# Kernel tuning notes

Hardware: AMD Instinct MI355X
Metric: run time of the kernel (lower is better)

Reference implementation:

```python
import jax, jax.numpy as jnp
import numpy as np
import math

DIM = 512      # vMF embedding dim
B = 512        # batch
K = 10         # sample_size
C = 8192       # num_classes
L = 0.7        # kappa_confidence
T_REJ = 32     # fixed rejection-sampling tries (acceptance ~0.7 per try)


def _vmf_logc(k, dim=DIM):
    # Approximate log normalizer from the paper (approximate_logc=True path).
    nm14 = (dim - 1) / 4.0
    nm12 = (dim - 1) / 2.0
    np12 = (dim + 1) / 2.0
    sqrtm = jnp.sqrt(nm12 * nm12 + k * k)
    sqrtp = jnp.sqrt(np12 * np12 + k * k)
    return nm14 * (jnp.log(nm12 + sqrtm) + jnp.log(nm12 + sqrtp)) - 0.5 * (sqrtm + sqrtp)


def _split(params):
    # params layout: [log_probs(1), means(DIM), hidden_ik(1)] (single component).
    means = params[..., 1:1 + DIM]
    hidden_ik = params[..., -1]
    mu = means / jnp.linalg.norm(means, axis=-1, keepdims=True)
    kappa = 1.0 / jnp.exp(hidden_ik)  # positive(x) = exp(x) parametrization
    return mu, kappa


def _vmf_sample(key, mu, kappa, n):
    # Wood's algorithm, vectorized over (b, n) with fixed-count rejection.
    b, d = mu.shape
    kap = kappa[:, None]  # (b,1)
    bb = (-2.0 * kap + jnp.sqrt(4.0 * kap * kap + (d - 1) ** 2)) / (d - 1)
    x0 = (1.0 - bb) / (1.0 + bb)
    cc = kap * x0 + (d - 1) * jnp.log(1.0 - x0 * x0)
    kz, ku, kv = jax.random.split(key, 3)
    z = jax.random.beta(kz, (d - 1) / 2.0, (d - 1) / 2.0, (T_REJ, b, n))
    w = (1.0 - (1.0 + bb) * z) / (1.0 - (1.0 - bb) * z)  # (T,b,n)
    u = jax.random.uniform(ku, (T_REJ, b, n), minval=1e-10)
    acc = kap * w + (d - 1) * jnp.log(1.0 - x0 * w) - cc >= jnp.log(u)
    idx = jnp.argmax(acc, axis=0)  # first accepted try
    w_sel = jnp.take_along_axis(w, idx[None], axis=0)[0]  # (b,n)
    v = jax.random.normal(kv, (b, n, d))
    v = v - jnp.einsum('bnd,bd->bn', v, mu)[..., None] * mu[:, None, :]
    v = v / jnp.linalg.norm(v, axis=-1, keepdims=True)
    sin_t = jnp.sqrt(jnp.clip(1.0 - w_sel * w_sel, 0.0))
    return w_sel[..., None] * mu[:, None, :] + sin_t[..., None] * v  # (b,n,d)


def setup_inputs() -> dict:
    key = jax.random.key(0)
    kp, kw, kl = jax.random.split(key, 3)
    # Input distribution parameters: random means, hidden_ik ~ log(1/kappa) with realistic kappa.
    parameters = jax.random.normal(kp, (B, DIM + 2), dtype=jnp.float32)
    kappa0 = L / (1.0 - L * L) * (DIM - 1) / math.sqrt(DIM)  # ~31
    parameters = parameters.at[:, -1].set(0.1 * parameters[:, -1] - math.log(kappa0))
    # Class weight, built exactly as in __init__ (non-deterministic target).
    means = jax.random.normal(kw, (C, DIM), dtype=jnp.float32) * (L / (1.0 - L * L) * (DIM - 1) / math.sqrt(DIM))
    norm = jnp.linalg.norm(means, axis=-1, keepdims=True)
    hidden_ik = jnp.log(1.0 / norm)  # ipositive = log
    weight = jnp.concatenate([jnp.zeros((C, 1), jnp.float32), means, hidden_ik], axis=-1)
    log_scale = jnp.asarray(2.773, dtype=jnp.float32)
    labels = jax.random.randint(kl, (B,), 0, C)
    return {"parameters": parameters, "weight": weight, "log_scale": log_scale, "labels": labels}


def reference(parameters, weight, log_scale, labels):
    scale = jnp.exp(log_scale)
    mu_x, kappa_x = _split(parameters)   # (b,d), (b,)
    mu_w, kappa_w = _split(weight)       # (c,d), (c,)
    sample = _vmf_sample(jax.random.key(42), mu_x, kappa_x, K)  # (b,K,d)
    sample = sample / jnp.linalg.norm(sample, axis=-1, keepdims=True)
    # logmls(b,k,c): samples have concentration k1=scale; since all means are unit,
    # ||k1*m1 + k2*m2|| = sqrt(k1^2 + k2^2 + 2*k1*k2*cos) -> single GEMM over d.
    cos = jnp.einsum('bkd,cd->bkc', sample, mu_w)
    k1 = scale
    k2 = kappa_w
    kk = jnp.sqrt(k1 * k1 + k2 * k2 + 2.0 * k1 * (k2 * cos))  # (b,K,c)
    logmls = _vmf_logc(k1) + _vmf_logc(k2)[None, None, :] - _vmf_logc(kk)
    neg_logden = jax.scipy.special.logsumexp(logmls, axis=2) - _vmf_logc(scale)  # (b,K)
    neg_lognum = scale * jnp.einsum('bd,bd->b', mu_x, mu_w[labels])
    losses = neg_logden.mean(axis=1) - neg_lognum  # (b,)
    b = parameters.shape[0]
    logits = jnp.zeros((b, C), parameters.dtype).at[jnp.arange(b), labels].set(-losses)
    return logits
```

## Files before the change

kernel.cpp:

```cpp
#include <hip/hip_runtime.h>
#include <stdint.h>

#define DIMD 512
#define BATCH 512
#define KSAMP 10
#define NCLS 8192
#define TREJ 32

typedef float f32x4 __attribute__((ext_vector_type(4)));
typedef long l2 __attribute__((ext_vector_type(2)));

__device__ inline uint64_t sm64(uint64_t x) {
  x += 0x9E3779B97F4A7C15ull;
  x = (x ^ (x >> 30)) * 0xBF58476D1CE4E5B9ull;
  x = (x ^ (x >> 27)) * 0x94D049BB133111EBull;
  return x ^ (x >> 31);
}
__device__ inline float u01(uint32_t u) {
  return ((float)u + 0.5f) * 2.3283064365386963e-10f;
}
__device__ inline float normal_from(uint64_t r) {
  float u1 = u01((uint32_t)(r >> 32));
  float u2 = u01((uint32_t)r);
  return sqrtf(-2.0f * __logf(u1)) * __cosf(6.28318530718f * u2);
}
__device__ inline float gamma255(uint64_t& ctr) {
  const float dg = 255.1666667f;
  const float cg = 0.02086730f;
  for (int i = 0; i < 16; i++) {
    uint64_t r = sm64(ctr++);
    float x = normal_from(r);
    float t = fmaf(cg, x, 1.0f);
    if (t <= 0.0f) continue;
    float v3 = t * t * t;
    uint64_t r2 = sm64(ctr++);
    float u3 = u01((uint32_t)(r2 >> 32));
    if (__logf(u3) < 0.5f * x * x + dg * (1.0f - v3 + __logf(v3))) return dg * v3;
  }
  return dg;
}
__device__ inline float wave_sum(float v) {
  #pragma unroll
  for (int o = 32; o > 0; o >>= 1) v += __shfl_down(v, o, 64);
  return __shfl(v, 0, 64);
}
__device__ inline float vmf_logc(float k) {
  float k2 = k * k;
  float sm = sqrtf(65280.25f + k2);
  float sp = sqrtf(65792.25f + k2);
  return 127.75f * (logf(255.5f + sm) + logf(255.5f + sp)) - 0.5f * (sm + sp);
}
__device__ inline void async16(const unsigned char* g, unsigned char* l) {
  __builtin_amdgcn_global_load_lds(
      (const __attribute__((address_space(1))) unsigned int*)g,
      (__attribute__((address_space(3))) unsigned int*)l, 16, 0, 0);
}
__device__ inline int2 pack_fp8x8(const float* v, float s) {
  int lo = 0, hi = 0;
  lo = __builtin_amdgcn_cvt_pk_fp8_f32(v[0] * s, v[1] * s, lo, false);
  lo = __builtin_amdgcn_cvt_pk_fp8_f32(v[2] * s, v[3] * s, lo, true);
  hi = __builtin_amdgcn_cvt_pk_fp8_f32(v[4] * s, v[5] * s, hi, false);
  hi = __builtin_amdgcn_cvt_pk_fp8_f32(v[6] * s, v[7] * s, hi, true);
  return make_int2(lo, hi);
}
__device__ inline int pk_off(int l) {
  return ((l >> 3) << 6) + ((l & 3) << 4) + (((l & 7) < 4) ? 0 : 8);
}

__global__ __launch_bounds__(256) void prep_sample(const float* __restrict__ weight,
                                                   const float* __restrict__ params,
                                                   const float* __restrict__ lscale,
                                                   unsigned char* __restrict__ muW8,
                                                   float4* __restrict__ cparams,
                                                   float* __restrict__ rowsum,
                                                   float4* __restrict__ out4,
                                                   unsigned char* __restrict__ Sb8) {
  int blk = blockIdx.x, tid = threadIdx.x;
  int wave = tid >> 6, lane = tid & 63;
  if (blk < 2048) {
    out4[(size_t)blk * 512 + tid]       = make_float4(0.f, 0.f, 0.f, 0.f);
    out4[(size_t)blk * 512 + 256 + tid] = make_float4(0.f, 0.f, 0.f, 0.f);
    if (blk < 20) rowsum[blk * 256 + tid] = 0.0f;

    int c = blk * 4 + wave;
    const float* wr = weight + (size_t)c * (DIMD + 2) + 1;
    float v[8];
    float n2 = 0.0f;
    #pragma unroll
    for (int j = 0; j < 8; j++) { v[j] = wr[lane * 8 + j]; n2 += v[j] * v[j]; }
    n2 = wave_sum(n2);
    float inv = rsqrtf(n2) * 16.0f;
    int2 pk = pack_fp8x8(v, inv);
    *(int2*)(muW8 + (size_t)c * 512 + pk_off(lane)) = pk;

    float hik = wr[DIMD];
    float kw = expf(-hik);
    float k1 = expf(lscale[0]);
    float lcw = vmf_logc(kw);
    float A2 = fmaf(k1, k1, kw * kw);
    float B2 = 2.0f * k1 * kw;
    const float X0 = 0.9238795f, X1 = 0.3826834f;
    int l3 = lane & 3;
    float Xj = (l3 == 0) ? X0 : (l3 == 1) ? X1 : (l3 == 2) ? -X1 : -X0;
    float gj = lcw - vmf_logc(sqrtf(fmaf(B2, Xj, A2)));
    float g0 = __shfl(gj, 0, 64), g1 = __shfl(gj, 1, 64);
    float g2 = __shfl(gj, 2, 64), g3 = __shfl(gj, 3, 64);
    if (lane == 0) {
      float b0 = 0.25f * (g0 + g1 + g2 + g3);
      float b1 = 0.5f * (X0 * (g0 - g3) + X1 * (g1 - g2));
      float b2 = 0.5f * 0.7071068f * ((g0 + g3) - (g1 + g2));
      float b3 = 0.5f * (X1 * (g0 - g3) - X0 * (g1 - g2));
      const float L2E = 1.4426950409f;
      const float S1 = 1.0f / 256.0f;
      float c0f = (b0 - b2) * L2E;
      float c1f = (b1 - 3.0f * b3) * L2E * S1;
      float c2f = (2.0f * b2) * L2E * S1 * S1;
      float c3f = (4.0f * b3) * L2E * S1 * S1 * S1;
      cparams[c] = make_float4(c0f, c1f, c2f, c3f);
    }
  } else {
    int row = (blk - 2048) * 4 + wave;
    int b = row / KSAMP;
    const float* pr = params + (size_t)b * (DIMD + 2) + 1;

    float mu[8];
    float n2 = 0.0f;
    #pragma unroll
    for (int j = 0; j < 8; j++) { mu[j] = pr[lane * 8 + j]; n2 += mu[j] * mu[j]; }
    n2 = wave_sum(n2);
    float invn = rsqrtf(n2);
    #pragma unroll
    for (int j = 0; j < 8; j++) mu[j] *= invn;

    float kap = __expf(-pr[DIMD]);
    float bb = (-2.0f * kap + sqrtf(fmaf(4.0f * kap, kap, 511.0f * 511.0f))) / 511.0f;
    float x0 = (1.0f - bb) / (1.0f + bb);
    float cc = kap * x0 + 511.0f * __logf(1.0f - x0 * x0);

    uint64_t ctr = (((uint64_t)(row + 1)) << 32) | ((uint64_t)lane << 8);
    float g1 = gamma255(ctr);
    float g2 = gamma255(ctr);
    float z = g1 / (g1 + g2);
    float wt = (1.0f - (1.0f + bb) * z) / (1.0f - (1.0f - bb) * z);
    uint64_t r = sm64(ctr++);
    float u = u01((uint32_t)(r >> 32));
    float lhs = kap * wt + 511.0f * __logf(1.0f - x0 * wt) - cc;
    bool acc = (lane < TREJ) && (lhs >= __logf(fmaxf(u, 1e-10f)));
    uint64_t mask = __ballot(acc);
    int sel = mask ? (__ffsll((unsigned long long)mask) - 1) : 0;
    float w = __shfl(wt, sel, 64);

    uint64_t cbase = (((uint64_t)(row + 1)) << 32) | 0x40000000ull;
    float v[8];
    #pragma unroll
    for (int j = 0; j < 8; j++) v[j] = normal_from(sm64(cbase + (uint64_t)(lane * 8 + j)));
    float d = 0.0f;
    #pragma unroll
    for (int j = 0; j < 8; j++) d += v[j] * mu[j];
    d = wave_sum(d);
    float t2 = 0.0f;
    #pragma unroll
    for (int j = 0; j < 8; j++) { v[j] -= d * mu[j]; t2 += v[j] * v[j]; }
    t2 = wave_sum(t2);
    float ivt = rsqrtf(t2);
    float st = sqrtf(fmaxf(0.0f, 1.0f - w * w)) * ivt;
    float sv[8];
    float s2 = 0.0f;
    #pragma unroll
    for (int j = 0; j < 8; j++) { sv[j] = fmaf(st, v[j], w * mu[j]); s2 += sv[j] * sv[j]; }
    s2 = wave_sum(s2);
    float is = rsqrtf(s2) * 16.0f;
    int2 pk = pack_fp8x8(sv, is);
    *(int2*)(Sb8 + (size_t)row * 512 + pk_off(lane)) = pk;
  }
}

__global__ __launch_bounds__(256, 2) void gemm_lse(const unsigned char* __restrict__ Sb8,
                                                   const unsigned char* __restrict__ Wb8,
                                                   const float4* __restrict__ cparams,
                                                   float* __restrict__ rowsum) {
  __shared__ __align__(16) unsigned char As[2][256 * 64];
  __shared__ __align__(16) unsigned char Bs[2][128 * 64];
  int tid = threadIdx.x;
  int lane = tid & 63, wave = tid >> 6;
  int tx = lane & 15, tz = lane >> 4;

  int id = blockIdx.x;
  int xcd = id & 7, lid = id >> 3;
  int c0 = (xcd * 8 + (lid & 7)) * 128;
  int r0 = (lid >> 3) * 256;

  int srow = (lane >> 2);
  int kg   = (lane & 3) ^ ((lane >> 3) & 3);
  int chA0 = wave * 4;
  int chB0 = wave * 2;

  f32x4 acc[4][8];
  #pragma unroll
  for (int i = 0; i < 4; i++)
    #pragma unroll
    for (int j = 0; j < 8; j++) acc[i][j] = (f32x4){0.f, 0.f, 0.f, 0.f};

  #pragma unroll
  for (int c = 0; c < 4; c++) {
    int ch = chA0 + c, rowi = ch * 16 + srow;
    async16(&Sb8[(size_t)(r0 + rowi) * 512 + kg * 16], &As[0][ch * 1024]);
  }
  #pragma unroll
  for (int c = 0; c < 2; c++) {
    int ch = chB0 + c, rowi = ch * 16 + srow;
    async16(&Wb8[(size_t)(c0 + rowi) * 512 + kg * 16], &Bs[0][ch * 1024]);
  }

  int p = 0;
  for (int kt = 0; kt < 512; kt += 64) {
    __syncthreads();
    if (kt + 64 < 512) {
      #pragma unroll
      for (int c = 0; c < 4; c++) {
        int ch = chA0 + c, rowi = ch * 16 + srow;
        async16(&Sb8[(size_t)(r0 + rowi) * 512 + kt + 64 + kg * 16], &As[p ^ 1][ch * 1024]);
      }
      #pragma unroll
      for (int c = 0; c < 2; c++) {
        int ch = chB0 + c, rowi = ch * 16 + srow;
        async16(&Wb8[(size_t)(c0 + rowi) * 512 + kt + 64 + kg * 16], &Bs[p ^ 1][ch * 1024]);
      }
    }
    l2 af[4], bf[8];
    int sA = tz ^ ((tx >> 1) & 3);
    #pragma unroll
    for (int mi = 0; mi < 4; mi++)
      af[mi] = *(const l2*)&As[p][(wave * 64 + mi * 16 + tx) * 64 + sA * 16];
    #pragma unroll
    for (int ni = 0; ni < 8; ni++)
      bf[ni] = *(const l2*)&Bs[p][(ni * 16 + tx) * 64 + sA * 16];
    #pragma unroll
    for (int mi = 0; mi < 4; mi++)
      #pragma unroll
      for (int ni = 0; ni < 8; ni++) {
        acc[mi][ni] = __builtin_amdgcn_mfma_f32_16x16x32_fp8_fp8(af[mi].x, bf[ni].x, acc[mi][ni], 0, 0, 0);
        acc[mi][ni] = __builtin_amdgcn_mfma_f32_16x16x32_fp8_fp8(af[mi].y, bf[ni].y, acc[mi][ni], 0, 0, 0);
      }
    p ^= 1;
  }

  float4 cp[8];
  #pragma unroll
  for (int ni = 0; ni < 8; ni++) cp[ni] = cparams[c0 + ni * 16 + tx];

  #pragma unroll
  for (int mi = 0; mi < 4; mi++) {
    #pragma unroll
    for (int reg = 0; reg < 4; reg++) {
      float s = 0.0f;
      #pragma unroll
      for (int ni = 0; ni < 8; ni++) {
        float cv = acc[mi][ni][reg];
        float g = fmaf(fmaf(fmaf(cp[ni].w, cv, cp[ni].z), cv, cp[ni].y), cv, cp[ni].x);
        s += exp2f(g);
      }
      #pragma unroll
      for (int o = 1; o < 16; o <<= 1) s += __shfl_xor(s, o, 64);
      if (tx == 0)
        atomicAdd(&rowsum[r0 + wave * 64 + mi * 16 + tz * 4 + reg], s);
    }
  }
}

__global__ __launch_bounds__(64) void finalize_kernel(const float* __restrict__ params,
                                                      const float* __restrict__ weight,
                                                      const float* __restrict__ rowsum,
                                                      const int* __restrict__ labels,
                                                      const float* __restrict__ lscale,
                                                      float* __restrict__ out) {
  int b = blockIdx.x;
  int lane = threadIdx.x;
  int lab = labels[b];
  const float* pr = params + (size_t)b * (DIMD + 2) + 1;
  const float* wr = weight + (size_t)lab * (DIMD + 2) + 1;
  float nx = 0.0f, nw = 0.0f, d = 0.0f;
  #pragma unroll
  for (int j = 0; j < 8; j++) {
    float xv = pr[j * 64 + lane];
    float wv = wr[j * 64 + lane];
    nx += xv * xv; nw += wv * wv; d += xv * wv;
  }
  nx = wave_sum(nx); nw = wave_sum(nw); d = wave_sum(d);
  if (lane == 0) {
    float k1 = expf(lscale[0]);
    float acc = 0.0f;
    #pragma unroll
    for (int k = 0; k < KSAMP; k++) acc += __logf(rowsum[b * KSAMP + k]);
    float loss = acc * (1.0f / KSAMP) - k1 * d * rsqrtf(nx) * rsqrtf(nw);
    out[(size_t)b * NCLS + lab] = -loss;
  }
}

extern "C" void kernel_launch(void* const* d_in, const int* in_sizes, int n_in,
                              void* d_out, int out_size, void* d_ws, size_t ws_size,
                              hipStream_t stream) {
  const float* params = (const float*)d_in[0];
  const float* weight = (const float*)d_in[1];
  const float* lscale = (const float*)d_in[2];
  const int*   labels = (const int*)d_in[3];
  float* out = (float*)d_out;
  char* ws = (char*)d_ws;

  unsigned char* muW8    = (unsigned char*)(ws);
  unsigned char* Sb8     = (unsigned char*)(ws + 4194304);
  float4*        cparams = (float4*)(ws + 6815744);
  float*         rowsum  = (float*)(ws + 6946816);

  hipLaunchKernelGGL(prep_sample, dim3(2048 + BATCH * KSAMP / 4), dim3(256), 0, stream,
                     weight, params, lscale, muW8, cparams, rowsum, (float4*)out, Sb8);
  hipLaunchKernelGGL(gemm_lse, dim3((NCLS / 128) * (BATCH * KSAMP / 256)), dim3(256), 0, stream,
                     Sb8, muW8, cparams, rowsum);
  hipLaunchKernelGGL(finalize_kernel, dim3(BATCH), dim3(64), 0, stream,
                     params, weight, rowsum, labels, lscale, out);
}
```

Measured before the change: 141.0 us.

## Replace async global-to-LDS loads with register-staged two-deep prefetch pipeline

The GEMM main loop no longer uses global_load_lds async copies. It prefetches K-chunks two iterations ahead into registers, writes them to the alternate LDS buffer after compute, and synchronises with a custom waitcnt plus barrier. The loop is fully unrolled, and the B fragments are loaded in two halves to cut live registers. The aim is to hide global latency behind MFMA work and avoid the vmcnt waits that async LDS loads force at the barrier. The cost is extra VGPRs for the staging buffers, which could hurt occupancy at 2 blocks per CU.

After: 140.6 us. No clear change (-0.3%).

```diff
diff --git a/kernel.cpp b/kernel.cpp
--- a/kernel.cpp
+++ b/kernel.cpp
@@ -50,11 +50,6 @@
   float sp = sqrtf(65792.25f + k2);
   return 127.75f * (logf(255.5f + sm) + logf(255.5f + sp)) - 0.5f * (sm + sp);
 }
-__device__ inline void async16(const unsigned char* g, unsigned char* l) {
-  __builtin_amdgcn_global_load_lds(
-      (const __attribute__((address_space(1))) unsigned int*)g,
-      (__attribute__((address_space(3))) unsigned int*)l, 16, 0, 0);
-}
 __device__ inline int2 pack_fp8x8(const float* v, float s) {
   int lo = 0, hi = 0;
   lo = __builtin_amdgcn_cvt_pk_fp8_f32(v[0] * s, v[1] * s, lo, false);
@@ -65,6 +60,9 @@
 }
 __device__ inline int pk_off(int l) {
   return ((l >> 3) << 6) + ((l & 3) << 4) + (((l & 7) < 4) ? 0 : 8);
+}
+__device__ inline void sync_lds() {
+  asm volatile("s_waitcnt lgkmcnt(0)\n\ts_barrier" ::: "memory");
 }
 
 __global__ __launch_bounds__(256) void prep_sample(const float* __restrict__ weight,
@@ -112,11 +110,9 @@
       float b3 = 0.5f * (X1 * (g0 - g3) - X0 * (g1 - g2));
       const float L2E = 1.4426950409f;
       const float S1 = 1.0f / 256.0f;
-      float c0f = (b0 - b2) * L2E;
-      float c1f = (b1 - 3.0f * b3) * L2E * S1;
-      float c2f = (2.0f * b2) * L2E * S1 * S1;
-      float c3f = (4.0f * b3) * L2E * S1 * S1 * S1;
-      cparams[c] = make_float4(c0f, c1f, c2f, c3f);
+      cparams[c] = make_float4((b0 - b2) * L2E, (b1 - 3.0f * b3) * L2E * S1,
+                               (2.0f * b2) * L2E * S1 * S1,
+                               (4.0f * b3) * L2E * S1 * S1 * S1);
     }
   } else {
     int row = (blk - 2048) * 4 + wave;
@@ -190,10 +186,19 @@
   int c0 = (xcd * 8 + (lid & 7)) * 128;
   int r0 = (lid >> 3) * 256;
 
-  int srow = (lane >> 2);
-  int kg   = (lane & 3) ^ ((lane >> 3) & 3);
-  int chA0 = wave * 4;
-  int chB0 = wave * 2;
+  int srow = lane >> 2;
+  int slot = lane & 3;
+  int kg = slot ^ ((srow >> 1) & 3);
+  const unsigned char* gA[4];
+  const unsigned char* gB[2];
+  #pragma unroll
+  for (int c = 0; c < 4; c++)
+    gA[c] = Sb8 + (size_t)(r0 + (wave * 4 + c) * 16 + srow) * 512 + kg * 16;
+  #pragma unroll
+  for (int c = 0; c < 2; c++)
+    gB[c] = Wb8 + (size_t)(c0 + (wave * 2 + c) * 16 + srow) * 512 + kg * 16;
+  int ldsAo = (wave * 4) * 1024 + lane * 16;
+  int ldsBo = (wave * 2) * 1024 + lane * 16;
 
   f32x4 acc[4][8];
   #pragma unroll
@@ -201,49 +206,68 @@
     #pragma unroll
     for (int j = 0; j < 8; j++) acc[i][j] = (f32x4){0.f, 0.f, 0.f, 0.f};
 
-  #pragma unroll
-  for (int c = 0; c < 4; c++) {
-    int ch = chA0 + c, rowi = ch * 16 + srow;
-    async16(&Sb8[(size_t)(r0 + rowi) * 512 + kg * 16], &As[0][ch * 1024]);
-  }
-  #pragma unroll
-  for (int c = 0; c < 2; c++) {
-    int ch = chB0 + c, rowi = ch * 16 + srow;
-    async16(&Wb8[(size_t)(c0 + rowi) * 512 + kg * 16], &Bs[0][ch * 1024]);
-  }
-
-  int p = 0;
-  for (int kt = 0; kt < 512; kt += 64) {
-    __syncthreads();
-    if (kt + 64 < 512) {
-      #pragma unroll
-      for (int c = 0; c < 4; c++) {
-        int ch = chA0 + c, rowi = ch * 16 + srow;
-        async16(&Sb8[(size_t)(r0 + rowi) * 512 + kt + 64 + kg * 16], &As[p ^ 1][ch * 1024]);
-      }
-      #pragma unroll
-      for (int c = 0; c < 2; c++) {
-        int ch = chB0 + c, rowi = ch * 16 + srow;
-        async16(&Wb8[(size_t)(c0 + rowi) * 512 + kt + 64 + kg * 16], &Bs[p ^ 1][ch * 1024]);
-      }
-    }
-    l2 af[4], bf[8];
-    int sA = tz ^ ((tx >> 1) & 3);
-    #pragma unroll
-    for (int mi = 0; mi < 4; mi++)
-      af[mi] = *(const l2*)&As[p][(wave * 64 + mi * 16 + tx) * 64 + sA * 16];
-    #pragma unroll
-    for (int ni = 0; ni < 8; ni++)
-      bf[ni] = *(const l2*)&Bs[p][(ni * 16 + tx) * 64 + sA * 16];
-    #pragma unroll
-    for (int mi = 0; mi < 4; mi++)
-      #pragma unroll
-      for (int ni = 0; ni < 8; ni++) {
-        acc[mi][ni] = __builtin_amdgcn_mfma_f32_16x16x32_fp8_fp8(af[mi].x, bf[ni].x, acc[mi][ni], 0, 0, 0);
-        acc[mi][ni] = __builtin_amdgcn_mfma_f32_16x16x32_fp8_fp8(af[mi].y, bf[ni].y, acc[mi][ni], 0, 0, 0);
-      }
-    p ^= 1;
-  }
+  int4 ar0[4], br0[2];
+  int4 ar1[4], br1[2];
+
+#define LOADCH(CI, AR, BR)                                   \
+  { AR[0] = *(const int4*)(gA[0] + (CI) * 64);               \
+    AR[1] = *(const int4*)(gA[1] + (CI) * 64);               \
+    AR[2] = *(const int4*)(gA[2] + (CI) * 64);               \
+    AR[3] = *(const int4*)(gA[3] + (CI) * 64);               \
+    BR[0] = *(const int4*)(gB[0] + (CI) * 64);               \
+    BR[1] = *(const int4*)(gB[1] + (CI) * 64); }
+
+#define WRITELDS(P, AR, BR)                                  \
+  { *(int4*)&As[P][ldsAo]        = AR[0];                    \
+    *(int4*)&As[P][ldsAo + 1024] = AR[1];                    \
+    *(int4*)&As[P][ldsAo + 2048] = AR[2];                    \
+    *(int4*)&As[P][ldsAo + 3072] = AR[3];                    \
+    *(int4*)&Bs[P][ldsBo]        = BR[0];                    \
+    *(int4*)&Bs[P][ldsBo + 1024] = BR[1]; }
+
+#define COMPUTE(P)                                                        \
+  { l2 af[4];                                                             \
+    int sA_ = tz ^ ((tx >> 1) & 3);                                       \
+    _Pragma("unroll")                                                     \
+    for (int mi = 0; mi < 4; mi++)                                        \
+      af[mi] = *(const l2*)&As[P][(wave * 64 + mi * 16 + tx) * 64 + sA_ * 16]; \
+    _Pragma("unroll")                                                     \
+    for (int h = 0; h < 2; h++) {                                         \
+      l2 bf[4];                                                           \
+      _Pragma("unroll")                                                   \
+      for (int ni = 0; ni < 4; ni++)                                      \
+        bf[ni] = *(const l2*)&Bs[P][((h * 4 + ni) * 16 + tx) * 64 + sA_ * 16]; \
+      _Pragma("unroll")                                                   \
+      for (int mi = 0; mi < 4; mi++)                                      \
+        _Pragma("unroll")                                                 \
+        for (int ni = 0; ni < 4; ni++)                                    \
+          acc[mi][h * 4 + ni] = __builtin_amdgcn_mfma_f32_16x16x32_fp8_fp8(af[mi].x, bf[ni].x, acc[mi][h * 4 + ni], 0, 0, 0); \
+      _Pragma("unroll")                                                   \
+      for (int mi = 0; mi < 4; mi++)                                      \
+        _Pragma("unroll")                                                 \
+        for (int ni = 0; ni < 4; ni++)                                    \
+          acc[mi][h * 4 + ni] = __builtin_amdgcn_mfma_f32_16x16x32_fp8_fp8(af[mi].y, bf[ni].y, acc[mi][h * 4 + ni], 0, 0, 0); \
+    } }
+
+  LOADCH(0, ar0, br0);
+  LOADCH(1, ar1, br1);
+  WRITELDS(0, ar0, br0);
+  sync_lds();
+
+#define GITER_EVEN(IT)                                       \
+  { if ((IT) + 2 < 8) LOADCH((IT) + 2, ar0, br0);            \
+    COMPUTE(0);                                              \
+    if ((IT) + 1 < 8) WRITELDS(1, ar1, br1);                 \
+    if ((IT) < 7) sync_lds(); }
+
+#define GITER_ODD(IT)                                        \
+  { if ((IT) + 2 < 8) LOADCH((IT) + 2, ar1, br1);            \
+    COMPUTE(1);                                              \
+    if ((IT) + 1 < 8) WRITELDS(0, ar0, br0);                 \
+    if ((IT) < 7) sync_lds(); }
+
+  GITER_EVEN(0) GITER_ODD(1) GITER_EVEN(2) GITER_ODD(3)
+  GITER_EVEN(4) GITER_ODD(5) GITER_EVEN(6) GITER_ODD(7)
 
   float4 cp[8];
   #pragma unroll
```
